# Optimization experiments

Measured on AMD Instinct MI355X. Metric: run time of the kernel, lower is better.

The kernel has to match this reference:

```python
import jax, jax.numpy as jnp
import numpy as np

B, N, IN_DIM, ATT_DIM = 2, 8192, 512, 512


def setup_inputs() -> dict:
    key = jax.random.key(0)
    k1, k2, k3, k4 = jax.random.split(key, 4)
    X = jax.random.normal(k1, (B, N, IN_DIM), dtype=jnp.float32)
    adj = jax.random.uniform(k2, (B, N, N), dtype=jnp.float32)
    mask = jnp.ones((B, N), dtype=jnp.float32)
    # Learned params (torch Linear stores W as (out,in); we store (in,out) for x @ W)
    Wqk = jax.random.normal(k3, (IN_DIM, 2 * ATT_DIM), dtype=jnp.float32) / np.sqrt(IN_DIM)
    Wv = jax.random.normal(k4, (IN_DIM, IN_DIM), dtype=jnp.float32) / np.sqrt(IN_DIM)
    return {"X": X, "adj": adj, "mask": mask, "Wqk": Wqk, "Wv": Wv}


def reference(X, adj, mask, Wqk, Wv):
    # q, k: (B, N, att_dim); v: (B, N, in_dim)
    qk = X @ Wqk
    q, k = jnp.split(qk, 2, axis=-1)
    v = X @ Wv
    att_dim = q.shape[-1]
    inv_scale = 1.0 / jnp.sqrt(jnp.float32(att_dim))
    # Original math: w_i = inv_scale * sum_j adj_ij * m_i * m_j * (q_i . k_j).
    # Since the rank-1 mask factors (m_i m_j), fold m_j into k and m_i into the row
    # score, avoiding a second materialized NxN tensor:
    k_m = k * mask[:, :, None]                       # (B, N, att_dim)
    agg = jnp.einsum("bij,bjd->bid", adj, k_m)       # (B, N, att_dim)
    w = inv_scale * mask * jnp.einsum("bid,bid->bi", q, agg)  # (B, N)
    # softmax over the bag dimension (dim=1), then scale v rows
    L = jax.nn.softmax(w, axis=1)[:, :, None] * v    # (B, N, in_dim)
    return L
```

## Files before the change

### kernel.cpp

```cpp
#include <hip/hip_runtime.h>
#include <math.h>

#define BB 2
#define NN 8192
#define DD 512

static const float INV_SCALE = 0.04419417382415922f;

typedef short s16x8 __attribute__((ext_vector_type(8)));
typedef unsigned short u16x8 __attribute__((ext_vector_type(8)));
typedef float f32x4 __attribute__((ext_vector_type(4)));

#define AS1 __attribute__((address_space(1)))
#define AS3 __attribute__((address_space(3)))

__device__ __forceinline__ unsigned short bfbits(__bf16 h) {
    return __builtin_bit_cast(unsigned short, h);
}

__device__ __forceinline__ float b2f(unsigned short u) {
    unsigned int x = (unsigned int)u << 16;
    return __builtin_bit_cast(float, x);
}

__device__ __forceinline__ void gll16(const void* g, void* l) {
    __builtin_amdgcn_global_load_lds((const AS1 unsigned int*)g, (AS3 unsigned int*)l, 16, 0, 0);
}

__device__ __forceinline__ f32x4 ntload4(const float* p) {
    return __builtin_nontemporal_load((const f32x4*)p);
}

__global__ __launch_bounds__(256) void convx_k(
    const float* __restrict__ X, unsigned short* __restrict__ Xhi,
    unsigned short* __restrict__ Xlo)
{
    long i = (long)blockIdx.x * 256 + threadIdx.x;
    float4 x = ((const float4*)X)[i];
    __bf16 h0 = (__bf16)x.x, h1 = (__bf16)x.y, h2 = (__bf16)x.z, h3 = (__bf16)x.w;
    ushort4 hi4 = make_ushort4(bfbits(h0), bfbits(h1), bfbits(h2), bfbits(h3));
    __bf16 l0 = (__bf16)(x.x - (float)h0), l1 = (__bf16)(x.y - (float)h1);
    __bf16 l2 = (__bf16)(x.z - (float)h2), l3 = (__bf16)(x.w - (float)h3);
    ushort4 lo4 = make_ushort4(bfbits(l0), bfbits(l1), bfbits(l2), bfbits(l3));
    ((ushort4*)Xhi)[i] = hi4;
    ((ushort4*)Xlo)[i] = lo4;
}

__global__ __launch_bounds__(256) void convw_k(
    const float* __restrict__ Wqk, const float* __restrict__ Wv,
    unsigned short* __restrict__ QTh, unsigned short* __restrict__ QTl,
    unsigned short* __restrict__ VTh, unsigned short* __restrict__ VTl)
{
    int i = blockIdx.x * 256 + threadIdx.x;
    float val; unsigned short *ph, *pl;
    if (i < 524288) {
        int n = i >> 9, k = i & 511;
        val = Wqk[k * 1024 + n]; ph = QTh + i; pl = QTl + i;
    } else {
        int o = i - 524288; int n = o >> 9, k = o & 511;
        val = Wv[k * 512 + n]; ph = VTh + o; pl = VTl + o;
    }
    __bf16 h = (__bf16)val;
    __bf16 l = (__bf16)(val - (float)h);
    *ph = bfbits(h); *pl = bfbits(l);
}


template <int EPI, int NT>
__global__ __launch_bounds__(256, 4) void mfma_gemm(
    const unsigned short* __restrict__ A0, const unsigned short* __restrict__ A1,
    const unsigned short* __restrict__ B0, const unsigned short* __restrict__ B1,
    float* __restrict__ C,
    float* __restrict__ q, float* __restrict__ km,
    unsigned short* __restrict__ qh, unsigned short* __restrict__ kmh,
    const float* __restrict__ mask, int N, int K)
{
    constexpr int BK = 32;
    constexpr int TILE_SH = 128 * BK;

    __shared__ unsigned short Asm[2 * TILE_SH];
    __shared__ unsigned short Bsm[2 * TILE_SH];

    const int t = threadIdx.x;
    const int wv = t >> 6, lane = t & 63;
    const int wm = wv >> 1, wn = wv & 1;
    const long m0 = blockIdx.x * 128;
    const int n0 = blockIdx.y * 128;

    f32x4 acc[4][4];
#pragma unroll
    for (int i = 0; i < 4; ++i)
#pragma unroll
        for (int j = 0; j < 4; ++j) acc[i][j] = {0.f, 0.f, 0.f, 0.f};

    const int swz = ((lane & 3) ^ ((lane >> 3) & 3)) << 4;
    auto stageA = [&](int term, int k0, int buf) {
        const unsigned short* Ab = (term < 2) ? A0 : A1;
#pragma unroll
        for (int u = 0; u < 2; ++u) {
            int c = wv * 2 + u;
            int row = c * 16 + (lane >> 2);
            gll16((const char*)Ab + ((m0 + row) * (long)K + k0) * 2 + swz,
                  (char*)Asm + buf * (TILE_SH * 2) + c * 1024);
        }
    };
    auto stageB = [&](int term, int k0, int buf) {
        const unsigned short* Bb = (NT == 3 && term == 1) ? B1 : B0;
#pragma unroll
        for (int u = 0; u < 2; ++u) {
            int c = wv * 2 + u;
            int row = c * 16 + (lane >> 2);
            gll16((const char*)Bb + ((long)(n0 + row) * K + k0) * 2 + swz,
                  (char*)Bsm + buf * (TILE_SH * 2) + c * 1024);
        }
    };

    stageA(0, 0, 0);
    stageB(0, 0, 0);
    __syncthreads();

    const int NTILES = NT * (K / BK);
    int cur = 0, term = 0, k0 = 0;
    const int g = lane >> 4;

#pragma unroll 2
    for (int tt = 0; tt < NTILES; ++tt) {
        int k0n = k0 + BK, termn = term;
        if (k0n == K) { k0n = 0; ++termn; }
        const bool hasNext = (tt + 1 < NTILES);

        if (hasNext) {
            stageA(termn, k0n, cur ^ 1);
            stageB(termn, k0n, cur ^ 1);
        }

        s16x8 av[4], bv[4];
#pragma unroll
        for (int f = 0; f < 4; ++f) {
            int ra = wm * 64 + f * 16 + (lane & 15);
            int rb = wn * 64 + f * 16 + (lane & 15);
            av[f] = *(const s16x8*)(Asm + cur * TILE_SH + ra * BK
                     + ((g ^ ((ra >> 1) & 3)) << 3));
            bv[f] = *(const s16x8*)(Bsm + cur * TILE_SH + rb * BK
                     + ((g ^ ((rb >> 1) & 3)) << 3));
        }
#pragma unroll
        for (int fm = 0; fm < 4; ++fm)
#pragma unroll
            for (int fn = 0; fn < 4; ++fn)
                acc[fm][fn] = __builtin_amdgcn_mfma_f32_16x16x32_bf16(
                    av[fm], bv[fn], acc[fm][fn], 0, 0, 0);

        __syncthreads();
        cur ^= 1; term = termn; k0 = k0n;
    }

    const long rbase = m0 + wm * 64;
    const int cbase = n0 + wn * 64;

    if constexpr (EPI == 0) {
#pragma unroll
        for (int fm = 0; fm < 4; ++fm) {
            long rb = rbase + fm * 16 + ((lane >> 4) << 2);
#pragma unroll
            for (int fn = 0; fn < 4; ++fn) {
                int c = cbase + fn * 16 + (lane & 15);
#pragma unroll
                for (int j = 0; j < 4; ++j)
                    C[(rb + j) * (long)N + c] = acc[fm][fn][j];
            }
        }
    } else {
        const bool isq = (n0 < 512);
#pragma unroll
        for (int fm = 0; fm < 4; ++fm) {
            long rb = rbase + fm * 16 + ((lane >> 4) << 2);
#pragma unroll
            for (int fn = 0; fn < 4; ++fn) {
                int c = cbase + fn * 16 + (lane & 15);
                if (isq) {
#pragma unroll
                    for (int j = 0; j < 4; ++j) {
                        float val = acc[fm][fn][j];
                        q [(rb + j) * 512L + c] = val;
                        qh[(rb + j) * 512L + c] = bfbits((__bf16)val);
                    }
                } else {
                    int c2 = c - 512;
#pragma unroll
                    for (int j = 0; j < 4; ++j) {
                        float kv = acc[fm][fn][j] * mask[rb + j];
                        km [(rb + j) * 512L + c2] = kv;
                        kmh[(rb + j) * 512L + c2] = bfbits((__bf16)kv);
                    }
                }
            }
        }
    }
}

__global__ __launch_bounds__(256, 5) void sq_gemm(
    const unsigned short* __restrict__ qh,
    const unsigned short* __restrict__ kmh,
    const float* __restrict__ adj,
    float* __restrict__ w)
{
    constexpr int BK = 32;
    constexpr int TILE_SH = 128 * BK;

    __shared__ __align__(16) char smem[32768];
    unsigned short* Asm = (unsigned short*)smem;
    unsigned short* Bsm = (unsigned short*)(smem + 16384);
    unsigned short* Sh = (unsigned short*)smem;

    const int t = threadIdx.x;
    const int wv = t >> 6, lane = t & 63;
    const int wm = wv >> 1, wn = wv & 1;

    const int bid = (int)blockIdx.x;
    const int xcd = bid & 7, s = bid >> 3;
    const int z = s >> 9, r = s & 511;
    const int jj = r & 7, ii = (r >> 3) & 7, jhi = r >> 6;
    const int i_tile = xcd * 8 + ii;
    const int j_tile = jhi * 8 + jj;

    const long m0 = (long)z * NN + (long)i_tile * 128;
    const int n0 = j_tile * 128;
    const unsigned short* Bz = kmh + (long)z * NN * 512;

    f32x4 acc[4][4];
#pragma unroll
    for (int i = 0; i < 4; ++i)
#pragma unroll
        for (int j = 0; j < 4; ++j) acc[i][j] = {0.f, 0.f, 0.f, 0.f};

    const int swz = ((lane & 3) ^ ((lane >> 3) & 3)) << 4;
    auto stageA = [&](int k0, int buf) {
#pragma unroll
        for (int u = 0; u < 2; ++u) {
            int c = wv * 2 + u;
            int row = c * 16 + (lane >> 2);
            gll16((const char*)qh + ((m0 + row) * 512L + k0) * 2 + swz,
                  (char*)Asm + buf * (TILE_SH * 2) + c * 1024);
        }
    };
    auto stageB = [&](int k0, int buf) {
#pragma unroll
        for (int u = 0; u < 2; ++u) {
            int c = wv * 2 + u;
            int row = c * 16 + (lane >> 2);
            gll16((const char*)Bz + ((long)(n0 + row) * 512 + k0) * 2 + swz,
                  (char*)Bsm + buf * (TILE_SH * 2) + c * 1024);
        }
    };

    stageA(0, 0);
    stageB(0, 0);
    __syncthreads();

    const int g = lane >> 4;
#pragma unroll 2
    for (int tt = 0; tt < 16; ++tt) {
        const int cur = tt & 1;
        const bool hasNext = (tt + 1 < 16);
        if (hasNext) {
            stageA((tt + 1) * BK, cur ^ 1);
            stageB((tt + 1) * BK, cur ^ 1);
        }

        s16x8 av[4], bv[4];
#pragma unroll
        for (int f = 0; f < 4; ++f) {
            int ra = wm * 64 + f * 16 + (lane & 15);
            int rb = wn * 64 + f * 16 + (lane & 15);
            av[f] = *(const s16x8*)(Asm + cur * TILE_SH + ra * BK
                     + ((g ^ ((ra >> 1) & 3)) << 3));
            bv[f] = *(const s16x8*)(Bsm + cur * TILE_SH + rb * BK
                     + ((g ^ ((rb >> 1) & 3)) << 3));
        }
#pragma unroll
        for (int fm = 0; fm < 4; ++fm)
#pragma unroll
            for (int fn = 0; fn < 4; ++fn)
                acc[fm][fn] = __builtin_amdgcn_mfma_f32_16x16x32_bf16(
                    av[fm], bv[fn], acc[fm][fn], 0, 0, 0);

        __syncthreads();
    }

    const int g2 = lane >> 4;
#pragma unroll
    for (int fm = 0; fm < 4; ++fm) {
#pragma unroll
        for (int fn = 0; fn < 4; ++fn) {
            int c = wn * 64 + fn * 16 + (lane & 15);
            int slotx = ((((c >> 2) ^ (g2 << 2)) << 2) | (c & 3));
#pragma unroll
            for (int j = 0; j < 4; ++j) {
                int rr = wm * 64 + fm * 16 + (g2 << 2) + j;
                Sh[rr * 128 + slotx] = bfbits((__bf16)acc[fm][fn][j]);
            }
        }
    }
    __syncthreads();

    const float* adjZ = adj + (long)z * NN * NN;
    const int li0 = i_tile * 128;
    float* wz = w + (long)z * NN;

#pragma unroll 1
    for (int half = 0; half < 2; ++half) {
        f32x4 aj[8];
#pragma unroll
        for (int i = 0; i < 8; ++i) {
            int f = t + (half * 8 + i) * 256;
            int rr = f >> 5, c4 = f & 31;
            aj[i] = ntload4(adjZ + (long)(li0 + rr) * NN + n0 + c4 * 4);
        }
#pragma unroll
        for (int i = 0; i < 8; ++i) {
            int f = t + (half * 8 + i) * 256;
            int rr = f >> 5, c4 = f & 31;
            int ps = (c4 ^ (((rr >> 2) & 3) << 2)) << 2;
            ushort4 sb = *(const ushort4*)(Sh + rr * 128 + ps);
            float p = aj[i][0] * b2f(sb.x) + aj[i][1] * b2f(sb.y)
                    + aj[i][2] * b2f(sb.z) + aj[i][3] * b2f(sb.w);
            p += __shfl_xor(p, 1);  p += __shfl_xor(p, 2);
            p += __shfl_xor(p, 4);  p += __shfl_xor(p, 8);
            p += __shfl_xor(p, 16);
            if ((t & 31) == 0) atomicAdd(wz + li0 + rr, p);
        }
    }
}

__global__ __launch_bounds__(256) void fixup_k(
    float* __restrict__ w, const float* __restrict__ mask)
{
    int i = blockIdx.x * 256 + threadIdx.x;
    w[i] *= INV_SCALE * mask[i];
}

__global__ __launch_bounds__(256) void wmax_k(const float* __restrict__ w,
                                              float* __restrict__ wmax)
{
    const int b = blockIdx.x;
    const float* wr = w + (long)b * NN;
    const int t = threadIdx.x;
    float m = -3.4e38f;
    for (int i = t; i < NN; i += 256) m = fmaxf(m, wr[i]);
#pragma unroll
    for (int o = 32; o > 0; o >>= 1) m = fmaxf(m, __shfl_down(m, o));
    __shared__ float red[4];
    if ((t & 63) == 0) red[t >> 6] = m;
    __syncthreads();
    if (t == 0) wmax[b] = fmaxf(fmaxf(red[0], red[1]), fmaxf(red[2], red[3]));
}

__global__ __launch_bounds__(256) void select_k(
    const float* __restrict__ w, const float* __restrict__ wmax,
    int* __restrict__ count, int* __restrict__ cand)
{
    int i = blockIdx.x * 256 + threadIdx.x;
    int b = i >> 13;
    if (w[i] >= wmax[b] - 15.f) {
        int p = atomicAdd(count, 1);
        if (p < 128) cand[p] = i;
    }
}

__global__ __launch_bounds__(256) void refine_k(
    const float* __restrict__ q, const float* __restrict__ km,
    const float* __restrict__ adj, const int* __restrict__ cand,
    const int* __restrict__ count, float* __restrict__ partial)
{
    int y = blockIdx.y;
    int cnt = *count; if (cnt > 128) cnt = 128;
    if (y >= cnt) return;
    const int row = cand[y];
    const int b = row >> 13, r = row & 8191;
    const int x = blockIdx.x;
    const int t = threadIdx.x, w = t >> 6, l = t & 63;

    const float* qr = q + (long)row * 512 + l * 8;
    const float4 q0 = *(const float4*)qr;
    const float4 q1 = *(const float4*)(qr + 4);
    const float* kmB = km + ((long)b << 13) * 512;
    const float* adjR = adj + (((long)b << 13) + r) * 8192L;

    float acc = 0.f;
    const int jbase = x * 128 + w * 32;
    for (int i = 0; i < 32; ++i) {
        int j = jbase + i;
        const float* kr = kmB + (long)j * 512 + l * 8;
        const float4 k0 = *(const float4*)kr;
        const float4 k1 = *(const float4*)(kr + 4);
        float d = q0.x * k0.x + q0.y * k0.y + q0.z * k0.z + q0.w * k0.w
                + q1.x * k1.x + q1.y * k1.y + q1.z * k1.z + q1.w * k1.w;
#pragma unroll
        for (int o = 32; o > 0; o >>= 1) d += __shfl_down(d, o);
        if (l == 0) acc += adjR[j] * d;
    }
    __shared__ float red[4];
    if (l == 0) red[w] = acc;
    __syncthreads();
    if (t == 0) partial[y * 64 + x] = red[0] + red[1] + red[2] + red[3];
}

__global__ __launch_bounds__(128) void apply_k(
    const int* __restrict__ cand, const int* __restrict__ count,
    const float* __restrict__ partial, const float* __restrict__ mask,
    float* __restrict__ w)
{
    int t = threadIdx.x;
    int cnt = *count; if (cnt > 128) cnt = 128;
    if (t < cnt) {
        float s = 0.f;
        for (int x = 0; x < 64; ++x) s += partial[t * 64 + x];
        int row = cand[t];
        w[row] = s * INV_SCALE * mask[row];
    }
}

__global__ __launch_bounds__(1024) void softmax_k(
    const float* __restrict__ w, float* __restrict__ p)
{
    const int b = blockIdx.x;
    const float* wr = w + (long)b * NN;
    float* pr = p + (long)b * NN;
    const int t = threadIdx.x;
    __shared__ float red[16];
    __shared__ float bmax, bsum;

    float m = -3.4e38f;
    for (int i = t; i < NN; i += 1024) m = fmaxf(m, wr[i]);
#pragma unroll
    for (int o = 32; o > 0; o >>= 1) m = fmaxf(m, __shfl_down(m, o));
    if ((t & 63) == 0) red[t >> 6] = m;
    __syncthreads();
    if (t == 0) {
        float mm = red[0];
        for (int i = 1; i < 16; ++i) mm = fmaxf(mm, red[i]);
        bmax = mm;
    }
    __syncthreads();
    const float M = bmax;

    float s = 0.f;
    for (int i = t; i < NN; i += 1024) s += expf(wr[i] - M);
#pragma unroll
    for (int o = 32; o > 0; o >>= 1) s += __shfl_down(s, o);
    __syncthreads();
    if ((t & 63) == 0) red[t >> 6] = s;
    __syncthreads();
    if (t == 0) {
        float ss = 0.f;
        for (int i = 0; i < 16; ++i) ss += red[i];
        bsum = ss;
    }
    __syncthreads();
    const float invS = 1.f / bsum;
    for (int i = t; i < NN; i += 1024) pr[i] = expf(wr[i] - M) * invS;
}

__global__ __launch_bounds__(256) void scale_k(
    const float* __restrict__ v, const float* __restrict__ p,
    float* __restrict__ out)
{
    const long i = (long)blockIdx.x * 256 + threadIdx.x;
    const int row = (int)(i >> 7);
    const float pv = p[row];
    float4 vv = ((const float4*)v)[i];
    vv.x *= pv; vv.y *= pv; vv.z *= pv; vv.w *= pv;
    ((float4*)out)[i] = vv;
}

extern "C" void kernel_launch(void* const* d_in, const int* in_sizes, int n_in,
                              void* d_out, int out_size, void* d_ws, size_t ws_size,
                              hipStream_t stream)
{
    const float* X    = (const float*)d_in[0];
    const float* adj  = (const float*)d_in[1];
    const float* mask = (const float*)d_in[2];
    const float* Wqk  = (const float*)d_in[3];
    const float* Wv   = (const float*)d_in[4];
    float* out = (float*)d_out;

    char* ws = (char*)d_ws;
    const long SZB = 33554432;
    float* q_buf  = (float*)(ws);
    float* km_buf = (float*)(ws + SZB);
    float* v_buf  = (float*)(ws + 2 * SZB);
    unsigned short* Xhi = (unsigned short*)(ws + 3 * SZB);
    unsigned short* Xlo = Xhi + 8388608;
    unsigned short* qh  = (unsigned short*)(ws + 4 * SZB);
    unsigned short* kmh = qh + 8388608;
    unsigned short* QTh = kmh + 8388608;
    unsigned short* QTl = QTh + 524288;
    unsigned short* VTh = QTl + 524288;
    unsigned short* VTl = VTh + 262144;
    float* w_buf = (float*)(VTl + 262144);
    float* p_buf = w_buf + 16384;
    float* wmax  = p_buf + 16384;
    float* partial = wmax + 64;
    int* count = (int*)(partial + 8192);
    int* cand  = count + 64;

    hipError_t e0 = hipMemsetAsync(count, 0, 4, stream); (void)e0;
    hipError_t e1 = hipMemsetAsync(w_buf, 0, 16384 * 4, stream); (void)e1;

    convx_k<<<8192, 256, 0, stream>>>(X, Xhi, Xlo);
    convw_k<<<3072, 256, 0, stream>>>(Wqk, Wv, QTh, QTl, VTh, VTl);

    mfma_gemm<1, 3><<<dim3(128, 8, 1), 256, 0, stream>>>(
        Xhi, Xlo, QTh, QTl, nullptr, q_buf, km_buf, qh, kmh, mask, 1024, 512);

    mfma_gemm<0, 1><<<dim3(128, 4, 1), 256, 0, stream>>>(
        Xhi, nullptr, VTh, nullptr, v_buf, nullptr, nullptr, nullptr, nullptr,
        nullptr, 512, 512);

    sq_gemm<<<8192, 256, 0, stream>>>(qh, kmh, adj, w_buf);

    fixup_k<<<64, 256, 0, stream>>>(w_buf, mask);

    wmax_k<<<BB, 256, 0, stream>>>(w_buf, wmax);
    select_k<<<64, 256, 0, stream>>>(w_buf, wmax, count, cand);
    refine_k<<<dim3(64, 128, 1), 256, 0, stream>>>(q_buf, km_buf, adj, cand, count, partial);
    apply_k<<<1, 128, 0, stream>>>(cand, count, partial, mask, w_buf);

    softmax_k<<<BB, 1024, 0, stream>>>(w_buf, p_buf);
    scale_k<<<8192, 256, 0, stream>>>(v_buf, p_buf, out);
}
```

Before: 437.3 us.

## Drop full fp32 q projection; compute fp32 q only for candidate rows

The Q half of the projection is now a single-pass bf16 GEMM that writes only the bf16 q buffer. The fp32 q, previously needed only by the refinement step, is recomputed in fp32 for the up to 128 softmax-dominant candidate rows by a new small kernel. This removes the hi/lo split terms and the fp32 q stores for the Q half of the GEMM. In exchange the bf16-only q feeding the N×N scoring is less precise, which could change which rows get selected as candidates.

```diff
diff --git a/kernel.cpp b/kernel.cpp
--- a/kernel.cpp
+++ b/kernel.cpp
@@ -48,21 +48,23 @@
 
 __global__ __launch_bounds__(256) void convw_k(
     const float* __restrict__ Wqk, const float* __restrict__ Wv,
-    unsigned short* __restrict__ QTh, unsigned short* __restrict__ QTl,
-    unsigned short* __restrict__ VTh, unsigned short* __restrict__ VTl)
+    unsigned short* __restrict__ QTh, unsigned short* __restrict__ KTh,
+    unsigned short* __restrict__ KTl, unsigned short* __restrict__ VTh)
 {
     int i = blockIdx.x * 256 + threadIdx.x;
-    float val; unsigned short *ph, *pl;
-    if (i < 524288) {
+    if (i < 262144) {
         int n = i >> 9, k = i & 511;
-        val = Wqk[k * 1024 + n]; ph = QTh + i; pl = QTl + i;
+        QTh[i] = bfbits((__bf16)Wqk[k * 1024 + n]);
+    } else if (i < 524288) {
+        int o = i - 262144; int n = o >> 9, k = o & 511;
+        float val = Wqk[k * 1024 + 512 + n];
+        __bf16 h = (__bf16)val;
+        KTh[o] = bfbits(h);
+        KTl[o] = bfbits((__bf16)(val - (float)h));
     } else {
         int o = i - 524288; int n = o >> 9, k = o & 511;
-        val = Wv[k * 512 + n]; ph = VTh + o; pl = VTl + o;
-    }
-    __bf16 h = (__bf16)val;
-    __bf16 l = (__bf16)(val - (float)h);
-    *ph = bfbits(h); *pl = bfbits(l);
+        VTh[o] = bfbits((__bf16)Wv[k * 512 + n]);
+    }
 }
 
 
@@ -70,10 +72,9 @@
 __global__ __launch_bounds__(256, 4) void mfma_gemm(
     const unsigned short* __restrict__ A0, const unsigned short* __restrict__ A1,
     const unsigned short* __restrict__ B0, const unsigned short* __restrict__ B1,
-    float* __restrict__ C,
-    float* __restrict__ q, float* __restrict__ km,
-    unsigned short* __restrict__ qh, unsigned short* __restrict__ kmh,
-    const float* __restrict__ mask, int N, int K)
+    float* __restrict__ C, float* __restrict__ kmf,
+    unsigned short* __restrict__ ubuf, const float* __restrict__ mask,
+    int N, int K)
 {
     constexpr int BK = 32;
     constexpr int TILE_SH = 128 * BK;
@@ -158,42 +159,27 @@
     const long rbase = m0 + wm * 64;
     const int cbase = n0 + wn * 64;
 
-    if constexpr (EPI == 0) {
-#pragma unroll
-        for (int fm = 0; fm < 4; ++fm) {
-            long rb = rbase + fm * 16 + ((lane >> 4) << 2);
-#pragma unroll
-            for (int fn = 0; fn < 4; ++fn) {
-                int c = cbase + fn * 16 + (lane & 15);
+#pragma unroll
+    for (int fm = 0; fm < 4; ++fm) {
+        long rb = rbase + fm * 16 + ((lane >> 4) << 2);
+#pragma unroll
+        for (int fn = 0; fn < 4; ++fn) {
+            int c = cbase + fn * 16 + (lane & 15);
+            if constexpr (EPI == 0) {
 #pragma unroll
                 for (int j = 0; j < 4; ++j)
                     C[(rb + j) * (long)N + c] = acc[fm][fn][j];
-            }
-        }
-    } else {
-        const bool isq = (n0 < 512);
-#pragma unroll
-        for (int fm = 0; fm < 4; ++fm) {
-            long rb = rbase + fm * 16 + ((lane >> 4) << 2);
-#pragma unroll
-            for (int fn = 0; fn < 4; ++fn) {
-                int c = cbase + fn * 16 + (lane & 15);
-                if (isq) {
-#pragma unroll
-                    for (int j = 0; j < 4; ++j) {
-                        float val = acc[fm][fn][j];
-                        q [(rb + j) * 512L + c] = val;
-                        qh[(rb + j) * 512L + c] = bfbits((__bf16)val);
-                    }
-                } else {
-                    int c2 = c - 512;
-#pragma unroll
-                    for (int j = 0; j < 4; ++j) {
-                        float kv = acc[fm][fn][j] * mask[rb + j];
-                        km [(rb + j) * 512L + c2] = kv;
-                        kmh[(rb + j) * 512L + c2] = bfbits((__bf16)kv);
-                    }
+            } else if constexpr (EPI == 1) {
+#pragma unroll
+                for (int j = 0; j < 4; ++j) {
+                    float kv = acc[fm][fn][j] * mask[rb + j];
+                    kmf [(rb + j) * 512L + c] = kv;
+                    ubuf[(rb + j) * 512L + c] = bfbits((__bf16)kv);
                 }
+            } else {
+#pragma unroll
+                for (int j = 0; j < 4; ++j)
+                    ubuf[(rb + j) * 512L + c] = bfbits((__bf16)acc[fm][fn][j]);
             }
         }
     }
@@ -368,8 +354,32 @@
     }
 }
 
+__global__ __launch_bounds__(256) void qcand_k(
+    const float* __restrict__ X, const float* __restrict__ Wqk,
+    const int* __restrict__ cand, const int* __restrict__ count,
+    float* __restrict__ qcand)
+{
+    int y = blockIdx.x;
+    int cnt = *count; if (cnt > 128) cnt = 128;
+    if (y >= cnt) return;
+    const int row = cand[y];
+    const float* Xr = X + (long)row * 512;
+    const int t = threadIdx.x;
+    __shared__ float xs[512];
+    for (int k = t; k < 512; k += 256) xs[k] = Xr[k];
+    __syncthreads();
+    float a0 = 0.f, a1 = 0.f;
+    for (int k = 0; k < 512; ++k) {
+        float xv = xs[k];
+        a0 += xv * Wqk[k * 1024 + t];
+        a1 += xv * Wqk[k * 1024 + t + 256];
+    }
+    qcand[(long)y * 512 + t] = a0;
+    qcand[(long)y * 512 + t + 256] = a1;
+}
+
 __global__ __launch_bounds__(256) void refine_k(
-    const float* __restrict__ q, const float* __restrict__ km,
+    const float* __restrict__ qcand, const float* __restrict__ km,
     const float* __restrict__ adj, const int* __restrict__ cand,
     const int* __restrict__ count, float* __restrict__ partial)
 {
@@ -381,7 +391,7 @@
     const int x = blockIdx.x;
     const int t = threadIdx.x, w = t >> 6, l = t & 63;
 
-    const float* qr = q + (long)row * 512 + l * 8;
+    const float* qr = qcand + (long)y * 512 + l * 8;
     const float4 q0 = *(const float4*)qr;
     const float4 q1 = *(const float4*)(qr + 4);
     const float* kmB = km + ((long)b << 13) * 512;
@@ -487,36 +497,38 @@
 
     char* ws = (char*)d_ws;
     const long SZB = 33554432;
-    float* q_buf  = (float*)(ws);
-    float* km_buf = (float*)(ws + SZB);
-    float* v_buf  = (float*)(ws + 2 * SZB);
-    unsigned short* Xhi = (unsigned short*)(ws + 3 * SZB);
+    float* km_buf = (float*)(ws);
+    float* v_buf  = (float*)(ws + SZB);
+    unsigned short* Xhi = (unsigned short*)(ws + 2 * SZB);
     unsigned short* Xlo = Xhi + 8388608;
-    unsigned short* qh  = (unsigned short*)(ws + 4 * SZB);
+    unsigned short* qh  = (unsigned short*)(ws + 3 * SZB);
     unsigned short* kmh = qh + 8388608;
     unsigned short* QTh = kmh + 8388608;
-    unsigned short* QTl = QTh + 524288;
-    unsigned short* VTh = QTl + 524288;
-    unsigned short* VTl = VTh + 262144;
-    float* w_buf = (float*)(VTl + 262144);
+    unsigned short* KTh = QTh + 262144;
+    unsigned short* KTl = KTh + 262144;
+    unsigned short* VTh = KTl + 262144;
+    float* w_buf = (float*)(VTh + 262144);
     float* p_buf = w_buf + 16384;
     float* wmax  = p_buf + 16384;
     float* partial = wmax + 64;
-    int* count = (int*)(partial + 8192);
+    float* qcand = partial + 8192;
+    int* count = (int*)(qcand + 65536);
     int* cand  = count + 64;
 
     hipError_t e0 = hipMemsetAsync(count, 0, 4, stream); (void)e0;
     hipError_t e1 = hipMemsetAsync(w_buf, 0, 16384 * 4, stream); (void)e1;
 
     convx_k<<<8192, 256, 0, stream>>>(X, Xhi, Xlo);
-    convw_k<<<3072, 256, 0, stream>>>(Wqk, Wv, QTh, QTl, VTh, VTl);
-
-    mfma_gemm<1, 3><<<dim3(128, 8, 1), 256, 0, stream>>>(
-        Xhi, Xlo, QTh, QTl, nullptr, q_buf, km_buf, qh, kmh, mask, 1024, 512);
+    convw_k<<<3072, 256, 0, stream>>>(Wqk, Wv, QTh, KTh, KTl, VTh);
+
+    mfma_gemm<1, 3><<<dim3(128, 4, 1), 256, 0, stream>>>(
+        Xhi, Xlo, KTh, KTl, nullptr, km_buf, kmh, mask, 512, 512);
+
+    mfma_gemm<2, 1><<<dim3(128, 4, 1), 256, 0, stream>>>(
+        Xhi, nullptr, QTh, nullptr, nullptr, nullptr, qh, nullptr, 512, 512);
 
     mfma_gemm<0, 1><<<dim3(128, 4, 1), 256, 0, stream>>>(
-        Xhi, nullptr, VTh, nullptr, v_buf, nullptr, nullptr, nullptr, nullptr,
-        nullptr, 512, 512);
+        Xhi, nullptr, VTh, nullptr, v_buf, nullptr, nullptr, nullptr, 512, 512);
 
     sq_gemm<<<8192, 256, 0, stream>>>(qh, kmh, adj, w_buf);
 
@@ -524,7 +536,8 @@
 
     wmax_k<<<BB, 256, 0, stream>>>(w_buf, wmax);
     select_k<<<64, 256, 0, stream>>>(w_buf, wmax, count, cand);
-    refine_k<<<dim3(64, 128, 1), 256, 0, stream>>>(q_buf, km_buf, adj, cand, count, partial);
+    qcand_k<<<128, 256, 0, stream>>>(X, Wqk, cand, count, qcand);
+    refine_k<<<dim3(64, 128, 1), 256, 0, stream>>>(qcand, km_buf, adj, cand, count, partial);
     apply_k<<<1, 128, 0, stream>>>(cand, count, partial, mask, w_buf);
 
     softmax_k<<<BB, 1024, 0, stream>>>(w_buf, p_buf);
```

After: 446.6 us. 2.1% more time.
